# Kernel tuning notes

Hardware: AMD Instinct MI355X
Metric: run time of the kernel (lower is better)

## Reference

```python
import jax, jax.numpy as jnp
import numpy as np

N = 50000       # nodes
E = 800000      # edges before self-loops (avg degree 16)
D_IN = 128
D_OUT = 128
DELTA = 2.5     # scaler normalization
EPS = 1e-5      # batchnorm eps
NEG_SLOPE = 0.01  # LeakyReLU default


def _lin_init(k, fan_in, shape):
    s = 1.0 / np.sqrt(fan_in)
    return jax.random.uniform(k, shape, jnp.float32, -s, s)


def setup_inputs() -> dict:
    key = jax.random.key(0)
    ks = jax.random.split(key, 12)
    ndata = jax.random.normal(ks[0], (N, D_IN), jnp.float32)
    src = jax.random.randint(ks[1], (E,), 0, N, jnp.int32)
    dst = jax.random.randint(ks[2], (E,), 0, N, jnp.int32)
    # PNAConvTower.M : Linear(2*in, in)
    M_w = _lin_init(ks[3], 2 * D_IN, (2 * D_IN, D_IN))
    M_b = _lin_init(ks[4], 2 * D_IN, (D_IN,))
    # PNAConvTower.U : Linear((3 aggs * 2 scalers + 1)*in, out) = Linear(7*in, out)
    U_w = _lin_init(ks[5], 7 * D_IN, (7 * D_IN, D_OUT))
    U_b = _lin_init(ks[6], 7 * D_IN, (D_OUT,))
    bn_gamma = jnp.ones((D_OUT,), jnp.float32)
    bn_beta = jnp.zeros((D_OUT,), jnp.float32)
    # PNAConv mixing layer: Linear(out, out) + LeakyReLU
    mix_w = _lin_init(ks[7], D_OUT, (D_OUT, D_OUT))
    mix_b = _lin_init(ks[8], D_OUT, (D_OUT,))
    return dict(ndata=ndata, M_w=M_w, M_b=M_b, U_w=U_w, U_b=U_b,
                bn_gamma=bn_gamma, bn_beta=bn_beta, mix_w=mix_w, mix_b=mix_b,
                src=src, dst=dst)


def reference(ndata, M_w, M_b, U_w, U_b, bn_gamma, bn_beta, mix_w, mix_b, src, dst):
    n = ndata.shape[0]
    # dgl.add_self_loop: append (i, i) for every node
    loop = jnp.arange(n, dtype=src.dtype)
    s = jnp.concatenate([src, loop])
    d = jnp.concatenate([dst, loop])
    # per-edge message: M(cat[h_src, h_dst])
    msg = jnp.concatenate([ndata[s], ndata[d]], axis=-1) @ M_w + M_b  # (E+N, D_IN)
    # in-degree per destination (>=1 due to self loops)
    deg = jax.ops.segment_sum(jnp.ones(d.shape, jnp.float32), d, num_segments=n)  # (N,)
    mean_agg = jax.ops.segment_sum(msg, d, num_segments=n) / deg[:, None]
    max_agg = jax.ops.segment_max(msg, d, num_segments=n)
    # aggregators ['mean','max','mean'] concatenated along feature dim
    agg = jnp.concatenate([mean_agg, max_agg, mean_agg], axis=-1)  # (N, 3*D_IN)
    # scalers ['identity','amplification'] applied to the concatenation
    amp = (jnp.log(deg + 1.0) / DELTA)[:, None]
    h_neigh = jnp.concatenate([agg, agg * amp], axis=-1)  # (N, 6*D_IN)
    # post-transform U on cat[node_feat, h_neigh]
    h = jnp.concatenate([ndata, h_neigh], axis=-1) @ U_w + U_b  # (N, D_OUT)
    # BatchNorm1d (training-mode batch stats, biased var)
    mu = h.mean(axis=0)
    var = ((h - mu) ** 2).mean(axis=0)
    h = (h - mu) * jax.lax.rsqrt(var + EPS) * bn_gamma + bn_beta
    # mixing layer: Linear + LeakyReLU
    out = h @ mix_w + mix_b
    return jax.nn.leaky_relu(out, NEG_SLOPE)
```

## Files before the change

kernel.cpp:

```cpp
#include <hip/hip_runtime.h>
#include <hip/hip_bf16.h>

#define NN 50000
#define EE 800000
#define DD 128
#define NBLK_SCAN 196

typedef short bf8 __attribute__((ext_vector_type(8)));
typedef float f32x4 __attribute__((ext_vector_type(4)));

__device__ __forceinline__ unsigned short f2b(float f) {
  __hip_bfloat16 h = __float2bfloat16(f);
  return *reinterpret_cast<unsigned short*>(&h);
}

__device__ __forceinline__ bf8 mk_a(const float* __restrict__ p, float sc) {
  float4 x0 = *(const float4*)p;
  float4 x1 = *(const float4*)(p + 4);
  bf8 a;
  a[0] = (short)f2b(x0.x * sc); a[1] = (short)f2b(x0.y * sc);
  a[2] = (short)f2b(x0.z * sc); a[3] = (short)f2b(x0.w * sc);
  a[4] = (short)f2b(x1.x * sc); a[5] = (short)f2b(x1.y * sc);
  a[6] = (short)f2b(x1.z * sc); a[7] = (short)f2b(x1.w * sc);
  return a;
}

__global__ __launch_bounds__(256) void pack_all(
    const float* __restrict__ Mw, const float* __restrict__ Uw, const float* __restrict__ Mixw,
    unsigned short* __restrict__ Mp, unsigned short* __restrict__ Up,
    unsigned short* __restrict__ Xp, unsigned int* __restrict__ cnt,
    float* __restrict__ bns, float* __restrict__ bnq) {
  int gid = blockIdx.x * 256 + threadIdx.x;
  if (gid < NN) cnt[gid] = 0u;
  if (gid < DD) { bns[gid] = 0.f; bnq[gid] = 0.f; }
  if (gid < 32768) {
    int g = gid;
    int j = g & 7, l = (g >> 3) & 63, ct = (g >> 9) & 15, kt = g >> 13;
    int k = kt * 32 + ((l >> 4) << 3) + j;
    int c = ct * 16 + (l & 15);
    float v = (c < 128) ? Mw[k * DD + c] : Mw[(128 + k) * DD + (c - 128)];
    Mp[g] = f2b(v);
  } else if (gid < 32768 + 81920) {
    int g = gid - 32768;
    int j = g & 7, l = (g >> 3) & 63, ct = (g >> 9) & 7, kt = g >> 12;
    int k = kt * 32 + ((l >> 4) << 3) + j;
    int p = k >> 7, kk = k & 127;
    int c = ct * 16 + (l & 15);
    float v;
    switch (p) {
      case 0: v = Uw[kk * DD + c]; break;
      case 1: v = Uw[(128 + kk) * DD + c] + Uw[(384 + kk) * DD + c]; break;
      case 2: v = Uw[(512 + kk) * DD + c] + Uw[(768 + kk) * DD + c]; break;
      case 3: v = Uw[(256 + kk) * DD + c]; break;
      default: v = Uw[(640 + kk) * DD + c]; break;
    }
    Up[g] = f2b(v);
  } else if (gid < 131072) {
    int g = gid - 114688;
    int j = g & 7, l = (g >> 3) & 63, ct = (g >> 9) & 7, kt = g >> 12;
    int k = kt * 32 + ((l >> 4) << 3) + j;
    int c = ct * 16 + (l & 15);
    Xp[g] = f2b(Mixw[k * DD + c]);
  }
}

__global__ __launch_bounds__(256) void gemm_prep(
    const float* __restrict__ nd, const unsigned short* __restrict__ Mp,
    const float* __restrict__ Mb, float* __restrict__ A, float* __restrict__ Bv) {
  const int w = threadIdx.x >> 6, l = threadIdx.x & 63;
  const int half = w >> 1;
  const int row0 = blockIdx.x * 32 + (w & 1) * 16;
  const int rc = min(row0 + (l & 15), NN - 1);
  const int ko = (l >> 4) * 8;
  const bf8* B8 = (const bf8*)Mp;
  f32x4 zero = {0.f, 0.f, 0.f, 0.f};
  f32x4 acc[8];
  #pragma unroll
  for (int i = 0; i < 8; i++) acc[i] = zero;
  #pragma unroll
  for (int ks = 0; ks < 4; ks++) {
    bf8 a = mk_a(nd + (size_t)rc * DD + ks * 32 + ko, 1.f);
    #pragma unroll
    for (int ct = 0; ct < 8; ct++) {
      bf8 b = B8[(ks * 16 + half * 8 + ct) * 64 + l];
      acc[ct] = __builtin_amdgcn_mfma_f32_16x16x32_bf16(a, b, acc[ct], 0, 0, 0);
    }
  }
  const int rb = row0 + (l >> 4) * 4;
  float* outp = half ? Bv : A;
  #pragma unroll
  for (int ct = 0; ct < 8; ct++) {
    int c = ct * 16 + (l & 15);
    float bias = half ? Mb[c] : 0.f;
    #pragma unroll
    for (int jj = 0; jj < 4; jj++) {
      int rr = rb + jj;
      if (rr < NN) outp[(size_t)rr * DD + c] = acc[ct][jj] + bias;
    }
  }
}

__global__ __launch_bounds__(256) void deg_count(
    const int* __restrict__ dst, unsigned int* __restrict__ cnt) {
  int e = blockIdx.x * 256 + threadIdx.x;
  if (e < EE) atomicAdd(&cnt[dst[e]], 1u);
}

__global__ __launch_bounds__(256) void scan_blk(
    const unsigned int* __restrict__ cnt, unsigned int* __restrict__ loc,
    unsigned int* __restrict__ bsum) {
  __shared__ unsigned int sh[256];
  const int t = threadIdx.x;
  const int i = blockIdx.x * 256 + t;
  unsigned int v = (i < NN) ? cnt[i] : 0u;
  sh[t] = v;
  __syncthreads();
  for (int d = 1; d < 256; d <<= 1) {
    unsigned int u = (t >= d) ? sh[t - d] : 0u;
    __syncthreads();
    sh[t] += u;
    __syncthreads();
  }
  if (i < NN) loc[i] = sh[t] - v;
  if (t == 255) bsum[blockIdx.x] = sh[255];
}

__global__ __launch_bounds__(256) void scan_top(
    const unsigned int* __restrict__ bsum, unsigned int* __restrict__ bbase) {
  __shared__ unsigned int sh[256];
  const int t = threadIdx.x;
  unsigned int v = (t < NBLK_SCAN) ? bsum[t] : 0u;
  sh[t] = v;
  __syncthreads();
  for (int d = 1; d < 256; d <<= 1) {
    unsigned int u = (t >= d) ? sh[t - d] : 0u;
    __syncthreads();
    sh[t] += u;
    __syncthreads();
  }
  if (t < NBLK_SCAN) bbase[t] = sh[t] - v;
}

__global__ __launch_bounds__(256) void scan_fin(
    const unsigned int* __restrict__ loc, const unsigned int* __restrict__ bbase,
    unsigned int* __restrict__ off, unsigned int* __restrict__ cursor) {
  const int i = blockIdx.x * 256 + threadIdx.x;
  if (i < NN) {
    unsigned int o = loc[i] + bbase[blockIdx.x];
    off[i] = o; cursor[i] = o;
  }
  if (i == 0) off[NN] = EE;
}

__global__ __launch_bounds__(256) void fill_k(
    const int* __restrict__ src, const int* __restrict__ dst,
    unsigned int* __restrict__ cursor, unsigned int* __restrict__ eidx) {
  int e = blockIdx.x * 256 + threadIdx.x;
  if (e < EE) {
    unsigned int p = atomicAdd(&cursor[dst[e]], 1u);
    eidx[p] = (unsigned int)src[e];
  }
}

__global__ __launch_bounds__(256) void aggregate(
    const float* __restrict__ A, const float* __restrict__ Bv,
    const unsigned int* __restrict__ off, const unsigned int* __restrict__ eidx,
    float* __restrict__ S, float* __restrict__ Xm, float* __restrict__ amp) {
  int wave = threadIdx.x >> 6, lane = threadIdx.x & 63;
  int n = blockIdx.x * 4 + wave;
  if (n >= NN) return;
  unsigned int b0 = off[n], b1 = off[n + 1];
  float2 sum = ((const float2*)(A + (size_t)n * DD))[lane];
  float2 mx = sum;
  for (unsigned int j0 = b0; j0 < b1; j0 += 64) {
    int m = (int)min(64u, b1 - j0);
    int myi = (lane < m) ? (int)eidx[j0 + lane] : 0;
    for (int j = 0; j < m; j++) {
      int sN = __shfl(myi, j);
      float2 a = ((const float2*)(A + (size_t)sN * DD))[lane];
      sum.x += a.x; sum.y += a.y;
      mx.x = fmaxf(mx.x, a.x); mx.y = fmaxf(mx.y, a.y);
    }
  }
  float degf = (float)(b1 - b0) + 1.f;
  float inv = 1.f / degf;
  float2 b = ((const float2*)(Bv + (size_t)n * DD))[lane];
  float2 sm = {sum.x * inv + b.x, sum.y * inv + b.y};
  float2 xm = {mx.x + b.x, mx.y + b.y};
  ((float2*)(S + (size_t)n * DD))[lane] = sm;
  ((float2*)(Xm + (size_t)n * DD))[lane] = xm;
  if (lane == 0) amp[n] = logf(degf + 1.f) * 0.4f;
}

__global__ __launch_bounds__(256) void gemm_u(
    const float* __restrict__ nd, const float* __restrict__ S, const float* __restrict__ Xm,
    const float* __restrict__ amp, const unsigned short* __restrict__ Up,
    const float* __restrict__ Ub, float* __restrict__ H,
    float* __restrict__ bns, float* __restrict__ bnq) {
  const int w = threadIdx.x >> 6, l = threadIdx.x & 63;
  const int row0 = blockIdx.x * 64 + w * 16;
  const int rc = min(row0 + (l & 15), NN - 1);
  const int ko = (l >> 4) * 8;
  const float av = amp[rc];
  const bf8* B8 = (const bf8*)Up;
  f32x4 zero = {0.f, 0.f, 0.f, 0.f};
  f32x4 acc[8];
  #pragma unroll
  for (int i = 0; i < 8; i++) acc[i] = zero;

  #pragma unroll 1
  for (int p = 0; p < 5; p++) {
    const float* sp = (p == 0) ? nd : (p < 3) ? S : Xm;
    const float sc = (p == 2 || p == 4) ? av : 1.f;
    const float* base = sp + (size_t)rc * DD + ko;
    #pragma unroll
    for (int q = 0; q < 4; q++) {
      bf8 a = mk_a(base + q * 32, sc);
      const int ks = p * 4 + q;
      #pragma unroll
      for (int ct = 0; ct < 8; ct++) {
        bf8 b = B8[(ks * 8 + ct) * 64 + l];
        acc[ct] = __builtin_amdgcn_mfma_f32_16x16x32_bf16(a, b, acc[ct], 0, 0, 0);
      }
    }
  }
  const int rb = row0 + (l >> 4) * 4;
  #pragma unroll
  for (int ct = 0; ct < 8; ct++) {
    int c = ct * 16 + (l & 15);
    float ub = Ub[c];
    float sS = 0.f, sQ = 0.f;
    #pragma unroll
    for (int jj = 0; jj < 4; jj++) {
      int rr = rb + jj;
      if (rr < NN) {
        float h = acc[ct][jj] + ub;
        H[(size_t)rr * DD + c] = h;
        sS += h; sQ += h * h;
      }
    }
    sS += __shfl_xor(sS, 16); sS += __shfl_xor(sS, 32);
    sQ += __shfl_xor(sQ, 16); sQ += __shfl_xor(sQ, 32);
    if ((l >> 4) == 0) {
      atomicAdd(bns + c, sS);
      atomicAdd(bnq + c, sQ);
    }
  }
}

__global__ __launch_bounds__(256) void gemm_final(
    const float* __restrict__ H, const float* __restrict__ bns, const float* __restrict__ bnq,
    const float* __restrict__ gamma, const float* __restrict__ beta,
    const unsigned short* __restrict__ Xp, const float* __restrict__ mixb,
    float* __restrict__ out) {
  const int w = threadIdx.x >> 6, l = threadIdx.x & 63;
  const int row0 = blockIdx.x * 64 + w * 16;
  const int rc = min(row0 + (l & 15), NN - 1);
  const int ko = (l >> 4) * 8;
  const bf8* B8 = (const bf8*)Xp;
  const float invN = 1.f / (float)NN;
  f32x4 zero = {0.f, 0.f, 0.f, 0.f};
  f32x4 acc[8];
  #pragma unroll
  for (int i = 0; i < 8; i++) acc[i] = zero;

  float aA[8], aO[8];
  #pragma unroll
  for (int ks = 0; ks < 4; ks++) {
    const int kch = ks * 32 + ko;
    if (ks == 0) {}
  }
  #pragma unroll
  for (int ks = 0; ks < 4; ks++) {
    const int kch = ks * 32 + ko;
    #pragma unroll
    for (int j = 0; j < 8; j++) {
      int c = kch + j;
      float mu = bns[c] * invN;
      float var = bnq[c] * invN - mu * mu;
      float a = gamma[c] * rsqrtf(var + 1e-5f);
      aA[j] = a; aO[j] = beta[c] - mu * a;
    }
    const float* p = H + (size_t)rc * DD + kch;
    float4 x0 = *(const float4*)p;
    float4 x1 = *(const float4*)(p + 4);
    bf8 a;
    a[0] = (short)f2b(x0.x * aA[0] + aO[0]); a[1] = (short)f2b(x0.y * aA[1] + aO[1]);
    a[2] = (short)f2b(x0.z * aA[2] + aO[2]); a[3] = (short)f2b(x0.w * aA[3] + aO[3]);
    a[4] = (short)f2b(x1.x * aA[4] + aO[4]); a[5] = (short)f2b(x1.y * aA[5] + aO[5]);
    a[6] = (short)f2b(x1.z * aA[6] + aO[6]); a[7] = (short)f2b(x1.w * aA[7] + aO[7]);
    #pragma unroll
    for (int ct = 0; ct < 8; ct++) {
      bf8 b = B8[(ks * 8 + ct) * 64 + l];
      acc[ct] = __builtin_amdgcn_mfma_f32_16x16x32_bf16(a, b, acc[ct], 0, 0, 0);
    }
  }
  const int rb = row0 + (l >> 4) * 4;
  #pragma unroll
  for (int ct = 0; ct < 8; ct++) {
    int c = ct * 16 + (l & 15);
    float mbv = mixb[c];
    #pragma unroll
    for (int jj = 0; jj < 4; jj++) {
      int rr = rb + jj;
      if (rr < NN) {
        float o = acc[ct][jj] + mbv;
        o = o > 0.f ? o : 0.01f * o;
        out[(size_t)rr * DD + c] = o;
      }
    }
  }
}

extern "C" void kernel_launch(void* const* d_in, const int* in_sizes, int n_in,
                              void* d_out, int out_size, void* d_ws, size_t ws_size,
                              hipStream_t stream) {
  const float* nd    = (const float*)d_in[0];
  const float* Mw    = (const float*)d_in[1];
  const float* Mb    = (const float*)d_in[2];
  const float* Uw    = (const float*)d_in[3];
  const float* Ub    = (const float*)d_in[4];
  const float* gamma = (const float*)d_in[5];
  const float* beta  = (const float*)d_in[6];
  const float* mixw  = (const float*)d_in[7];
  const float* mixb  = (const float*)d_in[8];
  const int* src = (const int*)d_in[9];
  const int* dst = (const int*)d_in[10];
  float* out = (float*)d_out;

  float* ws  = (float*)d_ws;
  float* A   = ws;
  float* Bv  = A + (size_t)NN * DD;
  float* S   = Bv + (size_t)NN * DD;
  float* Xm  = S + (size_t)NN * DD;
  float* H   = Xm + (size_t)NN * DD;
  float* amp = H + (size_t)NN * DD;
  float* bns = amp + NN;
  float* bnq = bns + DD;
  unsigned short* Mp = (unsigned short*)(bnq + DD);
  unsigned short* Up = Mp + 32768;
  unsigned short* Xp = Up + 81920;
  unsigned int* cnt    = (unsigned int*)(Xp + 16384);
  unsigned int* off    = cnt + NN;
  unsigned int* cursor = off + NN + 1;
  unsigned int* eidx   = cursor + NN;
  unsigned int* loc    = eidx + EE;
  unsigned int* bsum   = loc + NN;
  unsigned int* bbase  = bsum + 256;

  pack_all<<<512, 256, 0, stream>>>(Mw, Uw, mixw, Mp, Up, Xp, cnt, bns, bnq);
  gemm_prep<<<(NN + 31) / 32, 256, 0, stream>>>(nd, Mp, Mb, A, Bv);
  deg_count<<<(EE + 255) / 256, 256, 0, stream>>>(dst, cnt);
  scan_blk<<<NBLK_SCAN, 256, 0, stream>>>(cnt, loc, bsum);
  scan_top<<<1, 256, 0, stream>>>(bsum, bbase);
  scan_fin<<<NBLK_SCAN, 256, 0, stream>>>(loc, bbase, off, cursor);
  fill_k<<<(EE + 255) / 256, 256, 0, stream>>>(src, dst, cursor, eidx);
  aggregate<<<(NN + 3) / 4, 256, 0, stream>>>(A, Bv, off, eidx, S, Xm, amp);
  gemm_u<<<(NN + 63) / 64, 256, 0, stream>>>(nd, S, Xm, amp, Up, Ub, H, bns, bnq);
  gemm_final<<<(NN + 63) / 64, 256, 0, stream>>>(H, bns, bnq, gamma, beta, Xp, mixb, out);
}
```

Measured before the change: 479.7 us.

## Store intermediates in bf16 with MFMA-native tiled layouts and split amp accumulator

Converts the node features, the per-edge message table A, the aggregated S/Xm and H to bf16, written straight into the MFMA A-operand tile layout so the GEMMs load bf8 vectors directly. A new pack_nd kernel does the node-feature conversion. gemm_u keeps separate identity and amplification accumulators and applies the per-row amp scale in the epilogue instead of scaling inputs. This roughly halves gather bandwidth in aggregate and intermediate traffic, at the cost of bf16 rounding in the summed messages and the extra pack kernel.

```diff
diff --git a/kernel.cpp b/kernel.cpp
--- a/kernel.cpp
+++ b/kernel.cpp
@@ -4,6 +4,7 @@
 #define NN 50000
 #define EE 800000
 #define DD 128
+#define NT 3125
 #define NBLK_SCAN 196
 
 typedef short bf8 __attribute__((ext_vector_type(8)));
@@ -13,23 +14,18 @@
   __hip_bfloat16 h = __float2bfloat16(f);
   return *reinterpret_cast<unsigned short*>(&h);
 }
-
-__device__ __forceinline__ bf8 mk_a(const float* __restrict__ p, float sc) {
-  float4 x0 = *(const float4*)p;
-  float4 x1 = *(const float4*)(p + 4);
-  bf8 a;
-  a[0] = (short)f2b(x0.x * sc); a[1] = (short)f2b(x0.y * sc);
-  a[2] = (short)f2b(x0.z * sc); a[3] = (short)f2b(x0.w * sc);
-  a[4] = (short)f2b(x1.x * sc); a[5] = (short)f2b(x1.y * sc);
-  a[6] = (short)f2b(x1.z * sc); a[7] = (short)f2b(x1.w * sc);
-  return a;
+__device__ __forceinline__ float b2f_bits(unsigned short s) {
+  return __uint_as_float(((unsigned int)s) << 16);
+}
+__device__ __forceinline__ unsigned int pack2(float x, float y) {
+  return (unsigned int)f2b(x) | ((unsigned int)f2b(y) << 16);
 }
 
 __global__ __launch_bounds__(256) void pack_all(
     const float* __restrict__ Mw, const float* __restrict__ Uw, const float* __restrict__ Mixw,
-    unsigned short* __restrict__ Mp, unsigned short* __restrict__ Up,
-    unsigned short* __restrict__ Xp, unsigned int* __restrict__ cnt,
-    float* __restrict__ bns, float* __restrict__ bnq) {
+    unsigned short* __restrict__ Mp, unsigned short* __restrict__ Ui,
+    unsigned short* __restrict__ Ua, unsigned short* __restrict__ Xx,
+    unsigned int* __restrict__ cnt, float* __restrict__ bns, float* __restrict__ bnq) {
   int gid = blockIdx.x * 256 + threadIdx.x;
   if (gid < NN) cnt[gid] = 0u;
   if (gid < DD) { bns[gid] = 0.f; bnq[gid] = 0.f; }
@@ -40,38 +36,48 @@
     int c = ct * 16 + (l & 15);
     float v = (c < 128) ? Mw[k * DD + c] : Mw[(128 + k) * DD + (c - 128)];
     Mp[g] = f2b(v);
-  } else if (gid < 32768 + 81920) {
+  } else if (gid < 81920) {
     int g = gid - 32768;
     int j = g & 7, l = (g >> 3) & 63, ct = (g >> 9) & 7, kt = g >> 12;
     int k = kt * 32 + ((l >> 4) << 3) + j;
-    int p = k >> 7, kk = k & 127;
-    int c = ct * 16 + (l & 15);
-    float v;
-    switch (p) {
-      case 0: v = Uw[kk * DD + c]; break;
-      case 1: v = Uw[(128 + kk) * DD + c] + Uw[(384 + kk) * DD + c]; break;
-      case 2: v = Uw[(512 + kk) * DD + c] + Uw[(768 + kk) * DD + c]; break;
-      case 3: v = Uw[(256 + kk) * DD + c]; break;
-      default: v = Uw[(640 + kk) * DD + c]; break;
-    }
-    Up[g] = f2b(v);
+    int c = ct * 16 + (l & 15);
+    float v = Uw[k * DD + c];
+    if (k >= 128 && k < 256) v += Uw[(k + 256) * DD + c];
+    Ui[g] = f2b(v);
+  } else if (gid < 114688) {
+    int g = gid - 81920;
+    int j = g & 7, l = (g >> 3) & 63, ct = (g >> 9) & 7, kt = g >> 12;
+    int k = kt * 32 + ((l >> 4) << 3) + j;
+    int c = ct * 16 + (l & 15);
+    float v = Uw[(512 + k) * DD + c];
+    if (k < 128) v += Uw[(768 + k) * DD + c];
+    Ua[g] = f2b(v);
   } else if (gid < 131072) {
     int g = gid - 114688;
     int j = g & 7, l = (g >> 3) & 63, ct = (g >> 9) & 7, kt = g >> 12;
     int k = kt * 32 + ((l >> 4) << 3) + j;
     int c = ct * 16 + (l & 15);
-    Xp[g] = f2b(Mixw[k * DD + c]);
-  }
+    Xx[g] = f2b(Mixw[k * DD + c]);
+  }
+}
+
+__global__ __launch_bounds__(256) void pack_nd(
+    const float* __restrict__ nd, unsigned int* __restrict__ ndp) {
+  int gid = blockIdx.x * 256 + threadIdx.x;
+  int n = gid >> 6, ln = gid & 63;
+  float2 v = ((const float2*)nd)[gid];
+  int uidx = (n >> 4) * 1024 + (ln >> 4) * 256 + (((ln >> 2) & 3) * 16 + (n & 15)) * 4 + (ln & 3);
+  ndp[uidx] = pack2(v.x, v.y);
 }
 
 __global__ __launch_bounds__(256) void gemm_prep(
-    const float* __restrict__ nd, const unsigned short* __restrict__ Mp,
-    const float* __restrict__ Mb, float* __restrict__ A, float* __restrict__ Bv) {
+    const unsigned short* __restrict__ ndp, const unsigned short* __restrict__ Mp,
+    const float* __restrict__ Mb, unsigned short* __restrict__ A16, float* __restrict__ Bv) {
   const int w = threadIdx.x >> 6, l = threadIdx.x & 63;
-  const int half = w >> 1;
-  const int row0 = blockIdx.x * 32 + (w & 1) * 16;
-  const int rc = min(row0 + (l & 15), NN - 1);
-  const int ko = (l >> 4) * 8;
+  const int half = w >> 1, strip = w & 1;
+  const int row0 = blockIdx.x * 32 + strip * 16;
+  const int tile = min(blockIdx.x * 2 + strip, NT - 1);
+  const bf8* AP = (const bf8*)ndp;
   const bf8* B8 = (const bf8*)Mp;
   f32x4 zero = {0.f, 0.f, 0.f, 0.f};
   f32x4 acc[8];
@@ -79,7 +85,7 @@
   for (int i = 0; i < 8; i++) acc[i] = zero;
   #pragma unroll
   for (int ks = 0; ks < 4; ks++) {
-    bf8 a = mk_a(nd + (size_t)rc * DD + ks * 32 + ko, 1.f);
+    bf8 a = AP[tile * 256 + ks * 64 + l];
     #pragma unroll
     for (int ct = 0; ct < 8; ct++) {
       bf8 b = B8[(ks * 16 + half * 8 + ct) * 64 + l];
@@ -87,7 +93,6 @@
     }
   }
   const int rb = row0 + (l >> 4) * 4;
-  float* outp = half ? Bv : A;
   #pragma unroll
   for (int ct = 0; ct < 8; ct++) {
     int c = ct * 16 + (l & 15);
@@ -95,7 +100,11 @@
     #pragma unroll
     for (int jj = 0; jj < 4; jj++) {
       int rr = rb + jj;
-      if (rr < NN) outp[(size_t)rr * DD + c] = acc[ct][jj] + bias;
+      if (rr < NN) {
+        float v = acc[ct][jj] + bias;
+        if (half) Bv[(size_t)rr * DD + c] = v;
+        else      A16[(size_t)rr * DD + c] = f2b(v);
+      }
     }
   }
 }
@@ -163,79 +172,106 @@
 }
 
 __global__ __launch_bounds__(256) void aggregate(
-    const float* __restrict__ A, const float* __restrict__ Bv,
+    const unsigned short* __restrict__ A16, const float* __restrict__ Bv,
     const unsigned int* __restrict__ off, const unsigned int* __restrict__ eidx,
-    float* __restrict__ S, float* __restrict__ Xm, float* __restrict__ amp) {
-  int wave = threadIdx.x >> 6, lane = threadIdx.x & 63;
+    unsigned int* __restrict__ Sp, unsigned int* __restrict__ Xmp,
+    float* __restrict__ amp) {
+  int wave = threadIdx.x >> 6, ln = threadIdx.x & 63;
   int n = blockIdx.x * 4 + wave;
   if (n >= NN) return;
+  const unsigned int* Au = (const unsigned int*)A16;
   unsigned int b0 = off[n], b1 = off[n + 1];
-  float2 sum = ((const float2*)(A + (size_t)n * DD))[lane];
-  float2 mx = sum;
+  unsigned int su = Au[(size_t)n * 64 + ln];
+  float sx = b2f_bits((unsigned short)su), sy = b2f_bits((unsigned short)(su >> 16));
+  float sumx = sx, sumy = sy, mxx = sx, mxy = sy;
   for (unsigned int j0 = b0; j0 < b1; j0 += 64) {
     int m = (int)min(64u, b1 - j0);
-    int myi = (lane < m) ? (int)eidx[j0 + lane] : 0;
+    int myi = (ln < m) ? (int)eidx[j0 + ln] : 0;
     for (int j = 0; j < m; j++) {
       int sN = __shfl(myi, j);
-      float2 a = ((const float2*)(A + (size_t)sN * DD))[lane];
-      sum.x += a.x; sum.y += a.y;
-      mx.x = fmaxf(mx.x, a.x); mx.y = fmaxf(mx.y, a.y);
+      unsigned int au = Au[(size_t)sN * 64 + ln];
+      float ax = b2f_bits((unsigned short)au), ay = b2f_bits((unsigned short)(au >> 16));
+      sumx += ax; sumy += ay;
+      mxx = fmaxf(mxx, ax); mxy = fmaxf(mxy, ay);
     }
   }
   float degf = (float)(b1 - b0) + 1.f;
   float inv = 1.f / degf;
-  float2 b = ((const float2*)(Bv + (size_t)n * DD))[lane];
-  float2 sm = {sum.x * inv + b.x, sum.y * inv + b.y};
-  float2 xm = {mx.x + b.x, mx.y + b.y};
-  ((float2*)(S + (size_t)n * DD))[lane] = sm;
-  ((float2*)(Xm + (size_t)n * DD))[lane] = xm;
-  if (lane == 0) amp[n] = logf(degf + 1.f) * 0.4f;
+  float2 b = ((const float2*)(Bv + (size_t)n * DD))[ln];
+  float smx = sumx * inv + b.x, smy = sumy * inv + b.y;
+  float xmx = mxx + b.x, xmy = mxy + b.y;
+  int uidx = (n >> 4) * 1024 + (ln >> 4) * 256 + (((ln >> 2) & 3) * 16 + (n & 15)) * 4 + (ln & 3);
+  Sp[uidx] = pack2(smx, smy);
+  Xmp[uidx] = pack2(xmx, xmy);
+  if (ln == 0) amp[n] = logf(degf + 1.f) * 0.4f;
 }
 
 __global__ __launch_bounds__(256) void gemm_u(
-    const float* __restrict__ nd, const float* __restrict__ S, const float* __restrict__ Xm,
-    const float* __restrict__ amp, const unsigned short* __restrict__ Up,
-    const float* __restrict__ Ub, float* __restrict__ H,
+    const unsigned short* __restrict__ ndp, const unsigned short* __restrict__ Sp,
+    const unsigned short* __restrict__ Xmp, const float* __restrict__ amp,
+    const unsigned short* __restrict__ Ui, const unsigned short* __restrict__ Ua,
+    const float* __restrict__ Ub, unsigned short* __restrict__ Hp,
     float* __restrict__ bns, float* __restrict__ bnq) {
   const int w = threadIdx.x >> 6, l = threadIdx.x & 63;
   const int row0 = blockIdx.x * 64 + w * 16;
-  const int rc = min(row0 + (l & 15), NN - 1);
-  const int ko = (l >> 4) * 8;
-  const float av = amp[rc];
-  const bf8* B8 = (const bf8*)Up;
+  const int tile = min(blockIdx.x * 4 + w, NT - 1);
+  const bf8* ND = (const bf8*)ndp;
+  const bf8* SS = (const bf8*)Sp;
+  const bf8* XX = (const bf8*)Xmp;
+  const bf8* BI = (const bf8*)Ui;
+  const bf8* BA = (const bf8*)Ua;
   f32x4 zero = {0.f, 0.f, 0.f, 0.f};
-  f32x4 acc[8];
-  #pragma unroll
-  for (int i = 0; i < 8; i++) acc[i] = zero;
-
-  #pragma unroll 1
-  for (int p = 0; p < 5; p++) {
-    const float* sp = (p == 0) ? nd : (p < 3) ? S : Xm;
-    const float sc = (p == 2 || p == 4) ? av : 1.f;
-    const float* base = sp + (size_t)rc * DD + ko;
-    #pragma unroll
-    for (int q = 0; q < 4; q++) {
-      bf8 a = mk_a(base + q * 32, sc);
-      const int ks = p * 4 + q;
-      #pragma unroll
-      for (int ct = 0; ct < 8; ct++) {
-        bf8 b = B8[(ks * 8 + ct) * 64 + l];
-        acc[ct] = __builtin_amdgcn_mfma_f32_16x16x32_bf16(a, b, acc[ct], 0, 0, 0);
-      }
-    }
-  }
+  f32x4 accI[8], accA[8];
+  #pragma unroll
+  for (int i = 0; i < 8; i++) { accI[i] = zero; accA[i] = zero; }
+
+  #pragma unroll
+  for (int ks = 0; ks < 4; ks++) {
+    bf8 a = ND[tile * 256 + ks * 64 + l];
+    #pragma unroll
+    for (int ct = 0; ct < 8; ct++)
+      accI[ct] = __builtin_amdgcn_mfma_f32_16x16x32_bf16(a, BI[(ks * 8 + ct) * 64 + l], accI[ct], 0, 0, 0);
+  }
+  #pragma unroll
+  for (int ks = 0; ks < 4; ks++) {
+    bf8 a = SS[tile * 256 + ks * 64 + l];
+    #pragma unroll
+    for (int ct = 0; ct < 8; ct++)
+      accI[ct] = __builtin_amdgcn_mfma_f32_16x16x32_bf16(a, BI[((4 + ks) * 8 + ct) * 64 + l], accI[ct], 0, 0, 0);
+    #pragma unroll
+    for (int ct = 0; ct < 8; ct++)
+      accA[ct] = __builtin_amdgcn_mfma_f32_16x16x32_bf16(a, BA[(ks * 8 + ct) * 64 + l], accA[ct], 0, 0, 0);
+  }
+  #pragma unroll
+  for (int ks = 0; ks < 4; ks++) {
+    bf8 a = XX[tile * 256 + ks * 64 + l];
+    #pragma unroll
+    for (int ct = 0; ct < 8; ct++)
+      accI[ct] = __builtin_amdgcn_mfma_f32_16x16x32_bf16(a, BI[((8 + ks) * 8 + ct) * 64 + l], accI[ct], 0, 0, 0);
+    #pragma unroll
+    for (int ct = 0; ct < 8; ct++)
+      accA[ct] = __builtin_amdgcn_mfma_f32_16x16x32_bf16(a, BA[((4 + ks) * 8 + ct) * 64 + l], accA[ct], 0, 0, 0);
+  }
+
   const int rb = row0 + (l >> 4) * 4;
+  float ampv[4];
+  #pragma unroll
+  for (int jj = 0; jj < 4; jj++) ampv[jj] = amp[min(rb + jj, NN - 1)];
+
   #pragma unroll
   for (int ct = 0; ct < 8; ct++) {
     int c = ct * 16 + (l & 15);
     float ub = Ub[c];
+    int hks = ct >> 1;
+    int lpb = ((2 * ct + ((l >> 3) & 1)) & 3) * 16 + (l >> 4) * 4;
+    int hj = l & 7;
     float sS = 0.f, sQ = 0.f;
     #pragma unroll
     for (int jj = 0; jj < 4; jj++) {
       int rr = rb + jj;
       if (rr < NN) {
-        float h = acc[ct][jj] + ub;
-        H[(size_t)rr * DD + c] = h;
+        float h = accI[ct][jj] + ampv[jj] * accA[ct][jj] + ub;
+        Hp[(size_t)tile * 2048 + hks * 512 + (lpb + jj) * 8 + hj] = f2b(h);
         sS += h; sQ += h * h;
       }
     }
@@ -249,51 +285,39 @@
 }
 
 __global__ __launch_bounds__(256) void gemm_final(
-    const float* __restrict__ H, const float* __restrict__ bns, const float* __restrict__ bnq,
-    const float* __restrict__ gamma, const float* __restrict__ beta,
-    const unsigned short* __restrict__ Xp, const float* __restrict__ mixb,
-    float* __restrict__ out) {
+    const unsigned short* __restrict__ Hp, const float* __restrict__ bns,
+    const float* __restrict__ bnq, const float* __restrict__ gamma,
+    const float* __restrict__ beta, const unsigned short* __restrict__ Xx,
+    const float* __restrict__ mixb, float* __restrict__ out) {
   const int w = threadIdx.x >> 6, l = threadIdx.x & 63;
   const int row0 = blockIdx.x * 64 + w * 16;
-  const int rc = min(row0 + (l & 15), NN - 1);
-  const int ko = (l >> 4) * 8;
-  const bf8* B8 = (const bf8*)Xp;
+  const int tile = min(blockIdx.x * 4 + w, NT - 1);
+  const bf8* HP = (const bf8*)Hp;
+  const bf8* B8 = (const bf8*)Xx;
   const float invN = 1.f / (float)NN;
   f32x4 zero = {0.f, 0.f, 0.f, 0.f};
   f32x4 acc[8];
   #pragma unroll
   for (int i = 0; i < 8; i++) acc[i] = zero;
 
-  float aA[8], aO[8];
-  #pragma unroll
-  for (int ks = 0; ks < 4; ks++) {
-    const int kch = ks * 32 + ko;
-    if (ks == 0) {}
-  }
-  #pragma unroll
-  for (int ks = 0; ks < 4; ks++) {
-    const int kch = ks * 32 + ko;
+  #pragma unroll
+  for (int ks = 0; ks < 4; ks++) {
+    bf8 hp = HP[tile * 256 + ks * 64 + l];
+    const int cb = ks * 32 + (l >> 4) * 8;
+    bf8 a;
     #pragma unroll
     for (int j = 0; j < 8; j++) {
-      int c = kch + j;
+      int c = cb + j;
       float mu = bns[c] * invN;
       float var = bnq[c] * invN - mu * mu;
-      float a = gamma[c] * rsqrtf(var + 1e-5f);
-      aA[j] = a; aO[j] = beta[c] - mu * a;
-    }
-    const float* p = H + (size_t)rc * DD + kch;
-    float4 x0 = *(const float4*)p;
-    float4 x1 = *(const float4*)(p + 4);
-    bf8 a;
-    a[0] = (short)f2b(x0.x * aA[0] + aO[0]); a[1] = (short)f2b(x0.y * aA[1] + aO[1]);
-    a[2] = (short)f2b(x0.z * aA[2] + aO[2]); a[3] = (short)f2b(x0.w * aA[3] + aO[3]);
-    a[4] = (short)f2b(x1.x * aA[4] + aO[4]); a[5] = (short)f2b(x1.y * aA[5] + aO[5]);
-    a[6] = (short)f2b(x1.z * aA[6] + aO[6]); a[7] = (short)f2b(x1.w * aA[7] + aO[7]);
-    #pragma unroll
-    for (int ct = 0; ct < 8; ct++) {
-      bf8 b = B8[(ks * 8 + ct) * 64 + l];
-      acc[ct] = __builtin_amdgcn_mfma_f32_16x16x32_bf16(a, b, acc[ct], 0, 0, 0);
-    }
+      float sc = gamma[c] * rsqrtf(var + 1e-5f);
+      float ofs = beta[c] - mu * sc;
+      float h = b2f_bits((unsigned short)hp[j]);
+      a[j] = (short)f2b(fmaf(h, sc, ofs));
+    }
+    #pragma unroll
+    for (int ct = 0; ct < 8; ct++)
+      acc[ct] = __builtin_amdgcn_mfma_f32_16x16x32_bf16(a, B8[(ks * 8 + ct) * 64 + l], acc[ct], 0, 0, 0);
   }
   const int rb = row0 + (l >> 4) * 4;
   #pragma unroll
@@ -329,18 +353,20 @@
   float* out = (float*)d_out;
 
   float* ws  = (float*)d_ws;
-  float* A   = ws;
-  float* Bv  = A + (size_t)NN * DD;
-  float* S   = Bv + (size_t)NN * DD;
-  float* Xm  = S + (size_t)NN * DD;
-  float* H   = Xm + (size_t)NN * DD;
-  float* amp = H + (size_t)NN * DD;
+  float* Bv  = ws;
+  float* amp = Bv + (size_t)NN * DD;
   float* bns = amp + NN;
   float* bnq = bns + DD;
-  unsigned short* Mp = (unsigned short*)(bnq + DD);
-  unsigned short* Up = Mp + 32768;
-  unsigned short* Xp = Up + 81920;
-  unsigned int* cnt    = (unsigned int*)(Xp + 16384);
+  unsigned short* A16 = (unsigned short*)(bnq + DD);
+  unsigned short* ndp = A16 + (size_t)NN * DD;
+  unsigned short* Sp  = ndp + (size_t)NT * 2048;
+  unsigned short* Xmp = Sp + (size_t)NT * 2048;
+  unsigned short* Hp  = Xmp + (size_t)NT * 2048;
+  unsigned short* Mp  = Hp + (size_t)NT * 2048;
+  unsigned short* Ui  = Mp + 32768;
+  unsigned short* Ua  = Ui + 49152;
+  unsigned short* Xx  = Ua + 32768;
+  unsigned int* cnt    = (unsigned int*)(Xx + 16384);
   unsigned int* off    = cnt + NN;
   unsigned int* cursor = off + NN + 1;
   unsigned int* eidx   = cursor + NN;
@@ -348,14 +374,16 @@
   unsigned int* bsum   = loc + NN;
   unsigned int* bbase  = bsum + 256;
 
-  pack_all<<<512, 256, 0, stream>>>(Mw, Uw, mixw, Mp, Up, Xp, cnt, bns, bnq);
-  gemm_prep<<<(NN + 31) / 32, 256, 0, stream>>>(nd, Mp, Mb, A, Bv);
+  pack_all<<<512, 256, 0, stream>>>(Mw, Uw, mixw, Mp, Ui, Ua, Xx, cnt, bns, bnq);
+  pack_nd<<<12500, 256, 0, stream>>>(nd, (unsigned int*)ndp);
+  gemm_prep<<<(NN + 31) / 32, 256, 0, stream>>>(ndp, Mp, Mb, A16, Bv);
   deg_count<<<(EE + 255) / 256, 256, 0, stream>>>(dst, cnt);
   scan_blk<<<NBLK_SCAN, 256, 0, stream>>>(cnt, loc, bsum);
   scan_top<<<1, 256, 0, stream>>>(bsum, bbase);
   scan_fin<<<NBLK_SCAN, 256, 0, stream>>>(loc, bbase, off, cursor);
   fill_k<<<(EE + 255) / 256, 256, 0, stream>>>(src, dst, cursor, eidx);
-  aggregate<<<(NN + 3) / 4, 256, 0, stream>>>(A, Bv, off, eidx, S, Xm, amp);
-  gemm_u<<<(NN + 63) / 64, 256, 0, stream>>>(nd, S, Xm, amp, Up, Ub, H, bns, bnq);
-  gemm_final<<<(NN + 63) / 64, 256, 0, stream>>>(H, bns, bnq, gamma, beta, Xp, mixb, out);
-}
+  aggregate<<<(NN + 3) / 4, 256, 0, stream>>>(A16, Bv, off, eidx,
+                                              (unsigned int*)Sp, (unsigned int*)Xmp, amp);
+  gemm_u<<<(NN + 63) / 64, 256, 0, stream>>>(ndp, Sp, Xmp, amp, Ui, Ua, Ub, Hp, bns, bnq);
+  gemm_final<<<(NN + 63) / 64, 256, 0, stream>>>(Hp, bns, bnq, gamma, beta, Xx, mixb, out);
+}
```

New measurement: 435.6 us. 1.1x faster.
